# Optimization experiments

Hardware: AMD Instinct MI355X
Metric: run time of the kernel (lower is better)

## Reference

```python
import jax, jax.numpy as jnp
import numpy as np

B, C, N, H, K = 8, 256, 2048, 4, 64
HD = C // H
EPS = 1e-5
NEG = -1e30


def setup_inputs() -> dict:
    key = jax.random.key(0)
    ks = jax.random.split(key, 20)
    g = lambda i, shape, s=0.05: jax.random.normal(ks[i], shape, jnp.float32) * s
    lengths = jax.random.randint(ks[0], (B,), N // 2, N + 1).at[0].set(N).astype(jnp.int32)
    return dict(
        x=jax.random.normal(ks[1], (B, C, N), jnp.float32),
        lengths=lengths,
        WQ=g(2, (C, C)), WK=g(3, (C, C)), WV=g(4, (C, C)),
        in_proj_w=g(5, (3 * C, C)), in_proj_b=g(6, (3 * C,)),
        out_proj_w=g(7, (C, C)), out_proj_b=g(8, (C,)),
        ln1_w=1.0 + g(9, (C,)), ln1_b=g(10, (C,)),
        ln2_w=1.0 + g(11, (C,)), ln2_b=g(12, (C,)),
        ff1_w=g(13, (2 * C, C)), ff1_b=g(14, (2 * C,)),
        ff2_w=g(15, (C, 2 * C)), ff2_b=g(16, (C,)),
        proj_w=g(17, (K, C)), proj_b=g(18, (K,)),
    )


def _ln(x, w, b):
    m = jnp.mean(x, axis=-1, keepdims=True)
    v = jnp.var(x, axis=-1, keepdims=True)
    return (x - m) * jax.lax.rsqrt(v + EPS) * w + b


def reference(x, lengths, WQ, WK, WV, in_proj_w, in_proj_b, out_proj_w, out_proj_b,
              ln1_w, ln1_b, ln2_w, ln2_b, ff1_w, ff1_b, ff2_w, ff2_b, proj_w, proj_b):
    xt = jnp.transpose(x, (0, 2, 1))                      # [B,N,C]
    q = xt @ WQ
    k = xt @ WK
    v = xt @ WV
    valid = jnp.arange(N)[None, :] < lengths[:, None]     # [B,N]

    # nn.MultiheadAttention internal projections on (already projected) q,k,v
    Wq, Wk, Wv = jnp.split(in_proj_w, 3, axis=0)
    bq, bk, bv = jnp.split(in_proj_b, 3, axis=0)
    qh = (q @ Wq.T + bq).reshape(B, N, H, HD)
    kh = (k @ Wk.T + bk).reshape(B, N, H, HD)
    vh = (v @ Wv.T + bv).reshape(B, N, H, HD)
    scores = jnp.einsum('bqhd,bkhd->bhqk', qh, kh) / np.sqrt(HD).astype(np.float32)
    scores = jnp.where(valid[:, None, None, :], scores, NEG)  # mask padded keys
    attn = jax.nn.softmax(scores, axis=-1)
    o = jnp.einsum('bhqk,bkhd->bqhd', attn, vh).reshape(B, N, C)
    o = o @ out_proj_w.T + out_proj_b

    h1 = _ln(xt + o, ln1_w, ln1_b)
    ff = jax.nn.gelu(h1 @ ff1_w.T + ff1_b, approximate=False) @ ff2_w.T + ff2_b
    h2 = _ln(h1 + ff, ln2_w, ln2_b)
    logits = h2 @ proj_w.T + proj_b                       # [B,N,K]

    # softmax over the (valid) sequence positions, per cluster
    logits = jnp.where(valid[:, :, None], logits, NEG)
    sm = jax.nn.softmax(logits, axis=1)
    sm = jnp.where(valid[:, :, None], sm, 0.0)            # zero-pad like pad_sequence
    return jnp.transpose(sm, (0, 2, 1))                   # [B,K,N]
```

## Files before the change

### kernel.cpp

```cpp
#include <hip/hip_runtime.h>
#include <math.h>

constexpr int Bb = 8, Cc = 256, Nn = 2048, Hh = 4, HD = 64, KK = 64;
constexpr int Mm = Bb * Nn;
constexpr float NEG = -1e30f;

typedef unsigned short u16;
typedef __attribute__((ext_vector_type(8))) short bf16x8;
typedef __attribute__((ext_vector_type(4))) float f32x4;

static __device__ __forceinline__ u16 f2bf(float x) {
    union { float f; unsigned u; } v; v.f = x;
    const unsigned r = v.u + 0x7FFFu + ((v.u >> 16) & 1u);
    return (u16)(r >> 16);
}

#define SWZB(row, col) ((((row) * 128) + ((col) * 2)) ^ (((row) & 7) << 4))

__global__ __launch_bounds__(256) void xt_k(
    const float* __restrict__ x, u16* __restrict__ xb)
{
    __shared__ float Ts[64][65];
    const int tid = threadIdx.x;
    const int n0 = blockIdx.x * 64, c0 = blockIdx.y * 64, b = blockIdx.z;
    for (int c = tid; c < 1024; c += 256) {
        const int row = c >> 4, col = (c & 15) * 4;
        const float4 v = *(const float4*)(x + ((size_t)b * Cc + c0 + row) * Nn + n0 + col);
        Ts[row][col + 0] = v.x; Ts[row][col + 1] = v.y;
        Ts[row][col + 2] = v.z; Ts[row][col + 3] = v.w;
    }
    __syncthreads();
    for (int c = tid; c < 1024; c += 256) {
        const int nr = c >> 4, cc = (c & 15) * 4;
        const ushort4 o = make_ushort4(f2bf(Ts[cc + 0][nr]), f2bf(Ts[cc + 1][nr]),
                                       f2bf(Ts[cc + 2][nr]), f2bf(Ts[cc + 3][nr]));
        *(ushort4*)(xb + ((size_t)b * Nn + n0 + nr) * Cc + c0 + cc) = o;
    }
}

__global__ __launch_bounds__(256) void combine_w_k(
    const float* __restrict__ WQ, const float* __restrict__ WK,
    const float* __restrict__ WV, const float* __restrict__ inw,
    u16* __restrict__ cwb)
{
    __shared__ float ssub[256];
    const int row = blockIdx.x;
    const int part = row >> 8;
    const float* Wsrc = (part == 0) ? WQ : (part == 1) ? WK : WV;
    const int tid = threadIdx.x;
    ssub[tid] = inw[(size_t)row * 256 + tid];
    __syncthreads();
    float acc = 0.f;
    for (int c = 0; c < 256; c++)
        acc += Wsrc[(size_t)tid * 256 + c] * ssub[c];
    cwb[(size_t)row * 256 + tid] = f2bf(acc);
}

__global__ __launch_bounds__(256) void cvt4_k(
    const float* __restrict__ s0, u16* __restrict__ d0, int c0_,
    const float* __restrict__ s1, u16* __restrict__ d1, int c1_,
    const float* __restrict__ s2, u16* __restrict__ d2, int c2_,
    const float* __restrict__ s3, u16* __restrict__ d3, int c3_)
{
    const int q0 = c0_ >> 2, q1 = c1_ >> 2, q2 = c2_ >> 2, q3 = c3_ >> 2;
    const int total = q0 + q1 + q2 + q3;
    for (int i = blockIdx.x * 256 + threadIdx.x; i < total; i += gridDim.x * 256) {
        const float* s; u16* d; int idx = i;
        if (idx < q0)            { s = s0; d = d0; }
        else if ((idx -= q0) < q1) { s = s1; d = d1; }
        else if ((idx -= q1) < q2) { s = s2; d = d2; }
        else { idx -= q2;          s = s3; d = d3; }
        const float4 v = ((const float4*)s)[idx];
        ((ushort4*)d)[idx] = make_ushort4(f2bf(v.x), f2bf(v.y), f2bf(v.z), f2bf(v.w));
    }
}

template<int EPI>
__global__ __launch_bounds__(256) void gemm_mfma_k(
    const u16* __restrict__ A, const u16* __restrict__ W,
    const float* __restrict__ bias, const float* __restrict__ res,
    float* __restrict__ fout, u16* __restrict__ bout,
    u16* __restrict__ kout, u16* __restrict__ vtout,
    int Nout, int Kdim)
{
    __shared__ __align__(16) char AsB[128 * 128];
    __shared__ __align__(16) char WsB[64 * 128];

    const int tid = threadIdx.x;
    const int m0 = blockIdx.x * 128, n0 = blockIdx.y * 64;
    const int w = tid >> 6, l = tid & 63, g = l >> 4, li = l & 15;
    const int wm = w >> 1, wn = w & 1;

    f32x4 acc[4][2];
    #pragma unroll
    for (int mf = 0; mf < 4; mf++)
        #pragma unroll
        for (int nf = 0; nf < 2; nf++) acc[mf][nf] = f32x4{0.f, 0.f, 0.f, 0.f};

    for (int kt = 0; kt < Kdim; kt += 64) {
        __syncthreads();
        for (int c = tid; c < 1024; c += 256) {
            const int row = c >> 3, blk = c & 7;
            const uint4 v = *(const uint4*)(A + (size_t)(m0 + row) * Kdim + kt + blk * 8);
            *(uint4*)(AsB + SWZB(row, blk * 8)) = v;
        }
        for (int c = tid; c < 512; c += 256) {
            const int row = c >> 3, blk = c & 7;
            const uint4 v = *(const uint4*)(W + (size_t)(n0 + row) * Kdim + kt + blk * 8);
            *(uint4*)(WsB + SWZB(row, blk * 8)) = v;
        }
        __syncthreads();
        #pragma unroll
        for (int ks = 0; ks < 2; ks++) {
            bf16x8 af[4], bfr[2];
            #pragma unroll
            for (int mf = 0; mf < 4; mf++)
                af[mf] = *(const bf16x8*)(AsB + SWZB(wm * 64 + mf * 16 + li, ks * 32 + 8 * g));
            #pragma unroll
            for (int nf = 0; nf < 2; nf++)
                bfr[nf] = *(const bf16x8*)(WsB + SWZB(wn * 32 + nf * 16 + li, ks * 32 + 8 * g));
            #pragma unroll
            for (int mf = 0; mf < 4; mf++)
                #pragma unroll
                for (int nf = 0; nf < 2; nf++)
                    acc[mf][nf] = __builtin_amdgcn_mfma_f32_16x16x32_bf16(af[mf], bfr[nf], acc[mf][nf], 0, 0, 0);
        }
    }

    if (EPI == 0) {
        const int part = n0 >> 8;
        const int h    = (n0 >> 6) & 3;
        const int b    = m0 >> 11;
        const int bh   = b * 4 + h;
        #pragma unroll
        for (int mf = 0; mf < 4; mf++)
            #pragma unroll
            for (int nf = 0; nf < 2; nf++) {
                const int d  = wn * 32 + nf * 16 + li;
                const float bv = bias[n0 + d];
                const int nr0 = (m0 & (Nn - 1)) + wm * 64 + mf * 16 + 4 * g;
                if (part < 2) {
                    u16* dst = (part == 0) ? bout : kout;
                    #pragma unroll
                    for (int r = 0; r < 4; r++)
                        dst[((size_t)bh * Nn + nr0 + r) * 64 + d] = f2bf(acc[mf][nf][r] + bv);
                } else {
                    const ushort4 o = make_ushort4(
                        f2bf(acc[mf][nf][0] + bv), f2bf(acc[mf][nf][1] + bv),
                        f2bf(acc[mf][nf][2] + bv), f2bf(acc[mf][nf][3] + bv));
                    *(ushort4*)(vtout + ((size_t)bh * 64 + d) * Nn + nr0) = o;
                }
            }
    } else {
        #pragma unroll
        for (int mf = 0; mf < 4; mf++)
            #pragma unroll
            for (int nf = 0; nf < 2; nf++) {
                const int j = n0 + wn * 32 + nf * 16 + li;
                const float bv = bias[j];
                #pragma unroll
                for (int r = 0; r < 4; r++) {
                    const int m = m0 + wm * 64 + mf * 16 + 4 * g + r;
                    float v = acc[mf][nf][r] + bv;
                    if (EPI == 1) {
                        v += res[((size_t)(m >> 11) * Cc + j) * Nn + (m & (Nn - 1))];
                        fout[(size_t)m * Nout + j] = v;
                    } else if (EPI == 2) {
                        v = 0.5f * v * (1.0f + erff(v * 0.70710678118f));
                        bout[(size_t)m * Nout + j] = f2bf(v);
                    } else if (EPI == 3) {
                        v += res[(size_t)m * Nout + j];
                        fout[(size_t)m * Nout + j] = v;
                    } else {
                        fout[(size_t)m * Nout + j] = v;
                    }
                }
            }
    }
}

__global__ __launch_bounds__(256) void attn_mfma_k(
    const u16* __restrict__ qb, const u16* __restrict__ kb,
    const u16* __restrict__ vtb, const int* __restrict__ lengths,
    u16* __restrict__ outb)
{
    __shared__ __align__(16) char QsB[8192];
    __shared__ __align__(16) char KsB[8192];
    __shared__ __align__(16) char VtB[8192];
    __shared__ __align__(16) char PsB[8192];

    const int tid = threadIdx.x;
    const int qt = blockIdx.x;
    const int bh = blockIdx.y;
    const int b  = bh >> 2;
    const int len = lengths[b];
    const int w  = tid >> 6;
    const int l  = tid & 63;
    const int g  = l >> 4;
    const int li = l & 15;

    for (int c = tid; c < 512; c += 256) {
        const int row = c >> 3, blk = c & 7;
        const uint4 v = *(const uint4*)(qb + ((size_t)bh * Nn + qt * 64 + row) * 64 + blk * 8);
        *(uint4*)(QsB + SWZB(row, blk * 8)) = v;
    }
    __syncthreads();
    bf16x8 aq[2];
    #pragma unroll
    for (int ks = 0; ks < 2; ks++)
        aq[ks] = *(const bf16x8*)(QsB + SWZB(16 * w + li, 32 * ks + 8 * g));

    f32x4 oacc[4];
    #pragma unroll
    for (int df = 0; df < 4; df++) oacc[df] = f32x4{0.f, 0.f, 0.f, 0.f};
    float m_run[4], l_run[4];
    #pragma unroll
    for (int r = 0; r < 4; r++) { m_run[r] = NEG; l_run[r] = 0.f; }

    const int ktmax = (len + 63) >> 6;
    for (int kt = 0; kt < ktmax; ++kt) {
        __syncthreads();
        for (int c = tid; c < 512; c += 256) {
            const int row = c >> 3, blk = c & 7;
            const uint4 v = *(const uint4*)(kb + ((size_t)bh * Nn + kt * 64 + row) * 64 + blk * 8);
            *(uint4*)(KsB + SWZB(row, blk * 8)) = v;
        }
        for (int c = tid; c < 512; c += 256) {
            const int row = c >> 3, blk = c & 7;
            const uint4 v = *(const uint4*)(vtb + ((size_t)bh * 64 + row) * Nn + kt * 64 + blk * 8);
            *(uint4*)(VtB + SWZB(row, blk * 8)) = v;
        }
        __syncthreads();

        f32x4 s[4];
        #pragma unroll
        for (int cf = 0; cf < 4; cf++) {
            f32x4 z = f32x4{0.f, 0.f, 0.f, 0.f};
            #pragma unroll
            for (int ks = 0; ks < 2; ks++) {
                const bf16x8 bk = *(const bf16x8*)(KsB + SWZB(16 * cf + li, 32 * ks + 8 * g));
                z = __builtin_amdgcn_mfma_f32_16x16x32_bf16(aq[ks], bk, z, 0, 0, 0);
            }
            s[cf] = z;
        }
        float mt[4];
        #pragma unroll
        for (int r = 0; r < 4; r++) mt[r] = NEG;
        #pragma unroll
        for (int cf = 0; cf < 4; cf++) {
            const bool ok = (kt * 64 + 16 * cf + li) < len;
            #pragma unroll
            for (int r = 0; r < 4; r++) {
                const float v = ok ? s[cf][r] * 0.125f : NEG;
                s[cf][r] = v;
                mt[r] = fmaxf(mt[r], v);
            }
        }
        #pragma unroll
        for (int off = 1; off < 16; off <<= 1)
            #pragma unroll
            for (int r = 0; r < 4; r++) mt[r] = fmaxf(mt[r], __shfl_xor(mt[r], off));

        float f[4], sum[4];
        #pragma unroll
        for (int r = 0; r < 4; r++) {
            const float mn = fmaxf(m_run[r], mt[r]);
            f[r] = __expf(m_run[r] - mn);
            m_run[r] = mn;
            sum[r] = 0.f;
        }
        #pragma unroll
        for (int cf = 0; cf < 4; cf++)
            #pragma unroll
            for (int r = 0; r < 4; r++) {
                const float p = __expf(s[cf][r] - m_run[r]);
                sum[r] += p;
                const int row = 16 * w + 4 * g + r;
                *(u16*)(PsB + SWZB(row, 16 * cf + li)) = f2bf(p);
            }
        #pragma unroll
        for (int off = 1; off < 16; off <<= 1)
            #pragma unroll
            for (int r = 0; r < 4; r++) sum[r] += __shfl_xor(sum[r], off);
        #pragma unroll
        for (int r = 0; r < 4; r++) l_run[r] = l_run[r] * f[r] + sum[r];
        #pragma unroll
        for (int df = 0; df < 4; df++)
            #pragma unroll
            for (int r = 0; r < 4; r++) oacc[df][r] *= f[r];
        bf16x8 ap[2];
        #pragma unroll
        for (int ks = 0; ks < 2; ks++)
            ap[ks] = *(const bf16x8*)(PsB + SWZB(16 * w + li, 32 * ks + 8 * g));
        #pragma unroll
        for (int df = 0; df < 4; df++)
            #pragma unroll
            for (int ks = 0; ks < 2; ks++) {
                const bf16x8 bv = *(const bf16x8*)(VtB + SWZB(16 * df + li, 32 * ks + 8 * g));
                oacc[df] = __builtin_amdgcn_mfma_f32_16x16x32_bf16(ap[ks], bv, oacc[df], 0, 0, 0);
            }
    }
    #pragma unroll
    for (int r = 0; r < 4; r++) {
        const float inv = 1.f / l_run[r];
        const int qrow = qt * 64 + 16 * w + 4 * g + r;
        const size_t base = ((size_t)b * Nn + qrow) * Cc + (bh & 3) * 64;
        #pragma unroll
        for (int df = 0; df < 4; df++)
            outb[base + 16 * df + li] = f2bf(oacc[df][r] * inv);
    }
}

template<int MODE>
__global__ __launch_bounds__(256) void ln_k(
    const float* __restrict__ in, const float* __restrict__ w,
    const float* __restrict__ bc, float* __restrict__ outf,
    u16* __restrict__ outb)
{
    const int wave = threadIdx.x >> 6, lane = threadIdx.x & 63;
    const int row = blockIdx.x * 4 + wave;
    const float* p = in + (size_t)row * 256;
    const float v0 = p[lane], v1 = p[lane + 64], v2 = p[lane + 128], v3 = p[lane + 192];
    float s = v0 + v1 + v2 + v3;
    float s2 = v0 * v0 + v1 * v1 + v2 * v2 + v3 * v3;
    #pragma unroll
    for (int off = 32; off > 0; off >>= 1) {
        s  += __shfl_xor(s, off);
        s2 += __shfl_xor(s2, off);
    }
    const float mean = s * (1.f / 256.f);
    const float var  = s2 * (1.f / 256.f) - mean * mean;
    const float rstd = rsqrtf(var + 1e-5f);
    const float o0 = (v0 - mean) * rstd * w[lane]       + bc[lane];
    const float o1 = (v1 - mean) * rstd * w[lane + 64]  + bc[lane + 64];
    const float o2 = (v2 - mean) * rstd * w[lane + 128] + bc[lane + 128];
    const float o3 = (v3 - mean) * rstd * w[lane + 192] + bc[lane + 192];
    if (MODE == 0) {
        float* q = outf + (size_t)row * 256;
        q[lane] = o0; q[lane + 64] = o1; q[lane + 128] = o2; q[lane + 192] = o3;
    }
    u16* qb = outb + (size_t)row * 256;
    qb[lane] = f2bf(o0); qb[lane + 64] = f2bf(o1);
    qb[lane + 128] = f2bf(o2); qb[lane + 192] = f2bf(o3);
}

__global__ __launch_bounds__(256) void smax_k(
    const float* __restrict__ logits, const int* __restrict__ lengths,
    float* __restrict__ outp)
{
    __shared__ float red[8];
    const int bk = blockIdx.x;
    const int b = bk >> 6, kc = bk & 63;
    const int len = lengths[b];
    const int tid = threadIdx.x;
    const int lane = tid & 63, wv = tid >> 6;

    float m = NEG;
    for (int n = tid; n < len; n += 256)
        m = fmaxf(m, logits[((size_t)b * Nn + n) * KK + kc]);
    #pragma unroll
    for (int off = 32; off > 0; off >>= 1) m = fmaxf(m, __shfl_xor(m, off));
    if (lane == 0) red[wv] = m;
    __syncthreads();
    m = fmaxf(fmaxf(red[0], red[1]), fmaxf(red[2], red[3]));

    float s = 0.f;
    for (int n = tid; n < len; n += 256)
        s += __expf(logits[((size_t)b * Nn + n) * KK + kc] - m);
    #pragma unroll
    for (int off = 32; off > 0; off >>= 1) s += __shfl_xor(s, off);
    if (lane == 0) red[4 + wv] = s;
    __syncthreads();
    s = red[4] + red[5] + red[6] + red[7];
    const float inv = 1.f / s;

    for (int n = tid; n < Nn; n += 256) {
        float o = 0.f;
        if (n < len)
            o = __expf(logits[((size_t)b * Nn + n) * KK + kc] - m) * inv;
        outp[((size_t)b * KK + kc) * Nn + n] = o;
    }
}

extern "C" void kernel_launch(void* const* d_in, const int* in_sizes, int n_in,
                              void* d_out, int out_size, void* d_ws, size_t ws_size,
                              hipStream_t stream)
{
    (void)in_sizes; (void)n_in; (void)out_size; (void)ws_size;
    const float* x      = (const float*)d_in[0];
    const int*   lens   = (const int*)d_in[1];
    const float* WQ     = (const float*)d_in[2];
    const float* WK     = (const float*)d_in[3];
    const float* WV     = (const float*)d_in[4];
    const float* in_w   = (const float*)d_in[5];
    const float* in_b   = (const float*)d_in[6];
    const float* op_w   = (const float*)d_in[7];
    const float* op_b   = (const float*)d_in[8];
    const float* ln1w   = (const float*)d_in[9];
    const float* ln1b   = (const float*)d_in[10];
    const float* ln2w   = (const float*)d_in[11];
    const float* ln2b   = (const float*)d_in[12];
    const float* ff1w   = (const float*)d_in[13];
    const float* ff1b   = (const float*)d_in[14];
    const float* ff2w   = (const float*)d_in[15];
    const float* ff2b   = (const float*)d_in[16];
    const float* prw    = (const float*)d_in[17];
    const float* prb    = (const float*)d_in[18];
    float* out = (float*)d_out;

    char* ws = (char*)d_ws;
    const size_t MB = 1024 * 1024;
    u16*   xb    = (u16*)(ws + 0);
    u16*   cwb   = (u16*)(ws +  8 * MB);
    u16*   opwb  = (u16*)(ws +  9 * MB);
    u16*   f1wb  = (u16*)(ws + 10 * MB);
    u16*   f2wb  = (u16*)(ws + 11 * MB);
    u16*   prwb  = (u16*)(ws + 12 * MB);
    u16*   qbuf  = (u16*)(ws + 16 * MB);
    u16*   kbuf  = (u16*)(ws + 24 * MB);
    u16*   vtbuf = (u16*)(ws + 32 * MB);
    u16*   aob   = (u16*)(ws + 40 * MB);
    float* y1    = (float*)(ws + 48 * MB);
    float* h1    = (float*)(ws + 64 * MB);
    u16*   h1b   = (u16*)(ws + 80 * MB);
    u16*   ffmid = (u16*)(ws + 16 * MB);
    float* y2    = (float*)(ws + 32 * MB);
    u16*   h2b   = (u16*)(ws + 16 * MB);
    float* logits= (float*)(ws + 24 * MB);

    xt_k<<<dim3(Nn / 64, Cc / 64, Bb), 256, 0, stream>>>(x, xb);
    combine_w_k<<<768, 256, 0, stream>>>(WQ, WK, WV, in_w, cwb);
    cvt4_k<<<256, 256, 0, stream>>>(op_w, opwb, 256 * 256,
                                    ff1w, f1wb, 512 * 256,
                                    ff2w, f2wb, 256 * 512,
                                    prw,  prwb, 64 * 256);
    gemm_mfma_k<0><<<dim3(Mm / 128, 768 / 64), 256, 0, stream>>>(
        xb, cwb, in_b, nullptr, nullptr, qbuf, kbuf, vtbuf, 768, 256);
    attn_mfma_k<<<dim3(Nn / 64, Bb * Hh), 256, 0, stream>>>(qbuf, kbuf, vtbuf, lens, aob);
    gemm_mfma_k<1><<<dim3(Mm / 128, 256 / 64), 256, 0, stream>>>(
        aob, opwb, op_b, x, y1, nullptr, nullptr, nullptr, 256, 256);
    ln_k<0><<<Mm / 4, 256, 0, stream>>>(y1, ln1w, ln1b, h1, h1b);
    gemm_mfma_k<2><<<dim3(Mm / 128, 512 / 64), 256, 0, stream>>>(
        h1b, f1wb, ff1b, nullptr, nullptr, ffmid, nullptr, nullptr, 512, 256);
    gemm_mfma_k<3><<<dim3(Mm / 128, 256 / 64), 256, 0, stream>>>(
        ffmid, f2wb, ff2b, h1, y2, nullptr, nullptr, nullptr, 256, 512);
    ln_k<1><<<Mm / 4, 256, 0, stream>>>(y2, ln2w, ln2b, nullptr, h2b);
    gemm_mfma_k<4><<<dim3(Mm / 128, 64 / 64), 256, 0, stream>>>(
        h2b, prwb, prb, nullptr, logits, nullptr, nullptr, nullptr, 64, 256);
    smax_k<<<Bb * KK, 256, 0, stream>>>(logits, lens, out);
}
```

Measured before the change: 328.3 us.

## Transpose attention MFMA operands so each lane owns one query row

Swaps the A/B operands of the QK^T and PV MFMAs so the score tile is transposed. Each lane then holds one query row, which cuts the per-row max and sum reductions from four shuffle chains per lane to two shuffles. P is written to shared memory as packed 64-bit stores instead of scalar 16-bit stores, and the output is written as ushort4 vectors. The 1/sqrt(d) scale is folded into the Q projection epilogue, and key masking runs only on the last partial tile. This adds a small rounding difference from scaling Q before the bf16 conversion.

After: 313.3 us. 4.6% less time.

```diff
diff --git a/kernel.cpp b/kernel.cpp
--- a/kernel.cpp
+++ b/kernel.cpp
@@ -6,6 +6,7 @@
 constexpr float NEG = -1e30f;
 
 typedef unsigned short u16;
+typedef unsigned int u32;
 typedef __attribute__((ext_vector_type(8))) short bf16x8;
 typedef __attribute__((ext_vector_type(4))) float f32x4;
 
@@ -13,6 +14,9 @@
     union { float f; unsigned u; } v; v.f = x;
     const unsigned r = v.u + 0x7FFFu + ((v.u >> 16) & 1u);
     return (u16)(r >> 16);
+}
+static __device__ __forceinline__ u32 pk2(float a, float b) {
+    return (u32)f2bf(a) | ((u32)f2bf(b) << 16);
 }
 
 #define SWZB(row, col) ((((row) * 128) + ((col) * 2)) ^ (((row) & 7) << 4))
@@ -132,6 +136,7 @@
         const int h    = (n0 >> 6) & 3;
         const int b    = m0 >> 11;
         const int bh   = b * 4 + h;
+        const float sc = (part == 0) ? 0.125f : 1.0f;
         #pragma unroll
         for (int mf = 0; mf < 4; mf++)
             #pragma unroll
@@ -143,7 +148,7 @@
                     u16* dst = (part == 0) ? bout : kout;
                     #pragma unroll
                     for (int r = 0; r < 4; r++)
-                        dst[((size_t)bh * Nn + nr0 + r) * 64 + d] = f2bf(acc[mf][nf][r] + bv);
+                        dst[((size_t)bh * Nn + nr0 + r) * 64 + d] = f2bf((acc[mf][nf][r] + bv) * sc);
                 } else {
                     const ushort4 o = make_ushort4(
                         f2bf(acc[mf][nf][0] + bv), f2bf(acc[mf][nf][1] + bv),
@@ -187,7 +192,7 @@
     __shared__ __align__(16) char QsB[8192];
     __shared__ __align__(16) char KsB[8192];
     __shared__ __align__(16) char VtB[8192];
-    __shared__ __align__(16) char PsB[8192];
+    __shared__ __align__(16) char PtB[8192];
 
     const int tid = threadIdx.x;
     const int qt = blockIdx.x;
@@ -205,17 +210,15 @@
         *(uint4*)(QsB + SWZB(row, blk * 8)) = v;
     }
     __syncthreads();
-    bf16x8 aq[2];
+    bf16x8 bq[2];
     #pragma unroll
     for (int ks = 0; ks < 2; ks++)
-        aq[ks] = *(const bf16x8*)(QsB + SWZB(16 * w + li, 32 * ks + 8 * g));
+        bq[ks] = *(const bf16x8*)(QsB + SWZB(16 * w + li, 32 * ks + 8 * g));
 
     f32x4 oacc[4];
     #pragma unroll
     for (int df = 0; df < 4; df++) oacc[df] = f32x4{0.f, 0.f, 0.f, 0.f};
-    float m_run[4], l_run[4];
-    #pragma unroll
-    for (int r = 0; r < 4; r++) { m_run[r] = NEG; l_run[r] = 0.f; }
+    float m_run = NEG, l_run = 0.f;
 
     const int ktmax = (len + 63) >> 6;
     for (int kt = 0; kt < ktmax; ++kt) {
@@ -238,76 +241,71 @@
             f32x4 z = f32x4{0.f, 0.f, 0.f, 0.f};
             #pragma unroll
             for (int ks = 0; ks < 2; ks++) {
-                const bf16x8 bk = *(const bf16x8*)(KsB + SWZB(16 * cf + li, 32 * ks + 8 * g));
-                z = __builtin_amdgcn_mfma_f32_16x16x32_bf16(aq[ks], bk, z, 0, 0, 0);
+                const bf16x8 ak = *(const bf16x8*)(KsB + SWZB(16 * cf + li, 32 * ks + 8 * g));
+                z = __builtin_amdgcn_mfma_f32_16x16x32_bf16(ak, bq[ks], z, 0, 0, 0);
             }
             s[cf] = z;
         }
-        float mt[4];
-        #pragma unroll
-        for (int r = 0; r < 4; r++) mt[r] = NEG;
+        if (kt * 64 + 64 > len) {
+            #pragma unroll
+            for (int cf = 0; cf < 4; cf++)
+                #pragma unroll
+                for (int r = 0; r < 4; r++)
+                    if (kt * 64 + 16 * cf + 4 * g + r >= len) s[cf][r] = NEG;
+        }
+        float mt = s[0][0];
+        #pragma unroll
+        for (int cf = 0; cf < 4; cf++)
+            #pragma unroll
+            for (int r = 0; r < 4; r++) mt = fmaxf(mt, s[cf][r]);
+        mt = fmaxf(mt, __shfl_xor(mt, 16));
+        mt = fmaxf(mt, __shfl_xor(mt, 32));
+        const float mn = fmaxf(m_run, mt);
+        const float f = __expf(m_run - mn);
+        m_run = mn;
+        float sum = 0.f;
+        u32 pw[4][2];
         #pragma unroll
         for (int cf = 0; cf < 4; cf++) {
-            const bool ok = (kt * 64 + 16 * cf + li) < len;
-            #pragma unroll
-            for (int r = 0; r < 4; r++) {
-                const float v = ok ? s[cf][r] * 0.125f : NEG;
-                s[cf][r] = v;
-                mt[r] = fmaxf(mt[r], v);
+            const float p0 = __expf(s[cf][0] - mn);
+            const float p1 = __expf(s[cf][1] - mn);
+            const float p2 = __expf(s[cf][2] - mn);
+            const float p3 = __expf(s[cf][3] - mn);
+            sum += (p0 + p1) + (p2 + p3);
+            pw[cf][0] = pk2(p0, p1);
+            pw[cf][1] = pk2(p2, p3);
+        }
+        sum += __shfl_xor(sum, 16);
+        sum += __shfl_xor(sum, 32);
+        l_run = l_run * f + sum;
+        #pragma unroll
+        for (int cf = 0; cf < 4; cf++) {
+            uint2 pr; pr.x = pw[cf][0]; pr.y = pw[cf][1];
+            *(uint2*)(PtB + SWZB(16 * w + li, 16 * cf + 4 * g)) = pr;
+        }
+        #pragma unroll
+        for (int df = 0; df < 4; df++)
+            #pragma unroll
+            for (int r = 0; r < 4; r++) oacc[df][r] *= f;
+        bf16x8 bp[2];
+        #pragma unroll
+        for (int ks = 0; ks < 2; ks++)
+            bp[ks] = *(const bf16x8*)(PtB + SWZB(16 * w + li, 32 * ks + 8 * g));
+        #pragma unroll
+        for (int df = 0; df < 4; df++)
+            #pragma unroll
+            for (int ks = 0; ks < 2; ks++) {
+                const bf16x8 av = *(const bf16x8*)(VtB + SWZB(16 * df + li, 32 * ks + 8 * g));
+                oacc[df] = __builtin_amdgcn_mfma_f32_16x16x32_bf16(av, bp[ks], oacc[df], 0, 0, 0);
             }
-        }
-        #pragma unroll
-        for (int off = 1; off < 16; off <<= 1)
-            #pragma unroll
-            for (int r = 0; r < 4; r++) mt[r] = fmaxf(mt[r], __shfl_xor(mt[r], off));
-
-        float f[4], sum[4];
-        #pragma unroll
-        for (int r = 0; r < 4; r++) {
-            const float mn = fmaxf(m_run[r], mt[r]);
-            f[r] = __expf(m_run[r] - mn);
-            m_run[r] = mn;
-            sum[r] = 0.f;
-        }
-        #pragma unroll
-        for (int cf = 0; cf < 4; cf++)
-            #pragma unroll
-            for (int r = 0; r < 4; r++) {
-                const float p = __expf(s[cf][r] - m_run[r]);
-                sum[r] += p;
-                const int row = 16 * w + 4 * g + r;
-                *(u16*)(PsB + SWZB(row, 16 * cf + li)) = f2bf(p);
-            }
-        #pragma unroll
-        for (int off = 1; off < 16; off <<= 1)
-            #pragma unroll
-            for (int r = 0; r < 4; r++) sum[r] += __shfl_xor(sum[r], off);
-        #pragma unroll
-        for (int r = 0; r < 4; r++) l_run[r] = l_run[r] * f[r] + sum[r];
-        #pragma unroll
-        for (int df = 0; df < 4; df++)
-            #pragma unroll
-            for (int r = 0; r < 4; r++) oacc[df][r] *= f[r];
-        bf16x8 ap[2];
-        #pragma unroll
-        for (int ks = 0; ks < 2; ks++)
-            ap[ks] = *(const bf16x8*)(PsB + SWZB(16 * w + li, 32 * ks + 8 * g));
-        #pragma unroll
-        for (int df = 0; df < 4; df++)
-            #pragma unroll
-            for (int ks = 0; ks < 2; ks++) {
-                const bf16x8 bv = *(const bf16x8*)(VtB + SWZB(16 * df + li, 32 * ks + 8 * g));
-                oacc[df] = __builtin_amdgcn_mfma_f32_16x16x32_bf16(ap[ks], bv, oacc[df], 0, 0, 0);
-            }
-    }
-    #pragma unroll
-    for (int r = 0; r < 4; r++) {
-        const float inv = 1.f / l_run[r];
-        const int qrow = qt * 64 + 16 * w + 4 * g + r;
-        const size_t base = ((size_t)b * Nn + qrow) * Cc + (bh & 3) * 64;
-        #pragma unroll
-        for (int df = 0; df < 4; df++)
-            outb[base + 16 * df + li] = f2bf(oacc[df][r] * inv);
+    }
+    const float inv = 1.f / l_run;
+    const size_t base = ((size_t)b * Nn + qt * 64 + 16 * w + li) * Cc + (bh & 3) * 64;
+    #pragma unroll
+    for (int df = 0; df < 4; df++) {
+        const ushort4 o = make_ushort4(f2bf(oacc[df][0] * inv), f2bf(oacc[df][1] * inv),
+                                       f2bf(oacc[df][2] * inv), f2bf(oacc[df][3] * inv));
+        *(ushort4*)(outb + base + 16 * df + 4 * g) = o;
     }
 }
 
```
